# Kernel tuning notes

Measured on AMD Instinct MI355X. Metric: run time of the kernel, lower is better.

Reference implementation:

```python
import jax, jax.numpy as jnp
import numpy as np

DIM = 384; H = 56; W = 56; WS = 7; SHIFT = 3; NH = 12; B = 32
N = WS * WS                 # 49 tokens per window
NW = (H // WS) * (W // WS)  # 64 windows per image
HD = DIM // NH
EPS = 1e-5


def _rel_coords_table():
    c = np.arange(-(WS - 1), WS, dtype=np.float32)
    hh, ww = np.meshgrid(c, c, indexing='ij')
    t = np.stack([hh, ww], -1)[None]          # (1, 2*WS-1, 2*WS-1, 2)
    t = t / (WS - 1) * 8.0
    t = np.sign(t) * np.log2(np.abs(t) + 1.0) / 3.0
    return t.astype(np.float32)


def _rel_pos_index():
    coords = np.stack(np.meshgrid(np.arange(WS), np.arange(WS), indexing='ij'))  # (2,WS,WS)
    cf = coords.reshape(2, -1)
    rc = (cf[:, :, None] - cf[:, None, :]).transpose(1, 2, 0)  # (N,N,2)
    rc[..., 0] += WS - 1
    rc[..., 1] += WS - 1
    rc[..., 0] *= 2 * WS - 1
    return rc.sum(-1)  # (N,N) int


def _attn_mask():
    img = np.zeros((H, W))
    sl = [slice(0, -WS), slice(-WS, -SHIFT), slice(-SHIFT, None)]
    cnt = 0
    for hs in sl:
        for ws in sl:
            img[hs, ws] = cnt
            cnt += 1
    mw = img.reshape(H // WS, WS, W // WS, WS).transpose(0, 2, 1, 3).reshape(-1, N)
    diff = mw[:, None, :] - mw[:, :, None]  # (NW, N, N)
    return np.where(diff != 0, -100.0, 0.0).astype(np.float32)


_RCT = jnp.asarray(_rel_coords_table())
_RPI = jnp.asarray(_rel_pos_index().reshape(-1))
_MASK = jnp.asarray(_attn_mask())


def _layernorm(x, g, b):
    mu = jnp.mean(x, -1, keepdims=True)
    var = jnp.mean(jnp.square(x - mu), -1, keepdims=True)
    return (x - mu) * jax.lax.rsqrt(var + EPS) * g + b


def _forward(x, qkv_w, q_bias, v_bias, logit_scale, cpb_w1, cpb_b1, cpb_w2,
             proj_w, proj_b, norm1_g, norm1_b, norm2_g, norm2_b,
             mlp_w1, mlp_b1, mlp_w2, mlp_b2):
    shortcut = x
    xg = x.reshape(B, H, W, DIM)
    xg = jnp.roll(xg, shift=(-SHIFT, -SHIFT), axis=(1, 2))
    # window partition -> (B*NW, N, C)
    xw = xg.reshape(B, H // WS, WS, W // WS, WS, DIM).transpose(0, 1, 3, 2, 4, 5)
    xw = xw.reshape(B * NW, N, DIM)

    qkv_bias = jnp.concatenate([q_bias, jnp.zeros_like(v_bias), v_bias])
    qkv = xw @ qkv_w.T + qkv_bias                       # (Bw, N, 3C)
    qkv = qkv.reshape(B * NW, N, 3, NH, HD).transpose(2, 0, 3, 1, 4)
    q, k, v = qkv[0], qkv[1], qkv[2]                    # (Bw, NH, N, HD)

    qn = q / jnp.maximum(jnp.linalg.norm(q, axis=-1, keepdims=True), 1e-12)
    kn = k / jnp.maximum(jnp.linalg.norm(k, axis=-1, keepdims=True), 1e-12)
    attn = jnp.einsum('whnd,whmd->whnm', qn, kn)        # cosine attention
    scale = jnp.exp(jnp.minimum(logit_scale, jnp.log(100.0)))  # (NH,1,1)
    attn = attn * scale

    # CPB-MLP relative position bias
    bt = jnp.maximum(_RCT @ cpb_w1.T + cpb_b1, 0.0) @ cpb_w2.T  # (1,13,13,NH)
    bt = bt.reshape(-1, NH)
    rel_bias = bt[_RPI].reshape(N, N, NH).transpose(2, 0, 1)    # (NH,N,N)
    rel_bias = 16.0 * jax.nn.sigmoid(rel_bias)
    attn = attn + rel_bias[None]

    attn = attn.reshape(B, NW, NH, N, N) + _MASK[None, :, None]
    attn = jax.nn.softmax(attn, axis=-1).reshape(B * NW, NH, N, N)

    out = jnp.einsum('whnm,whmd->whnd', attn, v)        # (Bw, NH, N, HD)
    out = out.transpose(0, 2, 1, 3).reshape(B * NW, N, DIM)
    out = out @ proj_w.T + proj_b

    # window reverse + un-shift
    xg = out.reshape(B, H // WS, W // WS, WS, WS, DIM).transpose(0, 1, 3, 2, 4, 5)
    xg = xg.reshape(B, H, W, DIM)
    xg = jnp.roll(xg, shift=(SHIFT, SHIFT), axis=(1, 2))
    attn_out = xg.reshape(B, H * W, DIM)

    # SwinV2 post-norm residuals
    x1 = shortcut + _layernorm(attn_out, norm1_g, norm1_b)
    h = jax.nn.gelu(x1 @ mlp_w1.T + mlp_b1, approximate=False) @ mlp_w2.T + mlp_b2
    return x1 + _layernorm(h, norm2_g, norm2_b)


def setup_inputs() -> dict:
    key = jax.random.key(0)
    ks = jax.random.split(key, 8)
    s = 0.02
    return {
        'x': jax.random.normal(ks[0], (B, H * W, DIM), jnp.float32),
        'qkv_w': jax.random.normal(ks[1], (3 * DIM, DIM), jnp.float32) * s,
        'q_bias': jnp.zeros((DIM,), jnp.float32),
        'v_bias': jnp.zeros((DIM,), jnp.float32),
        'logit_scale': jnp.log(10.0 * jnp.ones((NH, 1, 1), jnp.float32)),
        'cpb_w1': jax.random.normal(ks[2], (512, 2), jnp.float32) * s,
        'cpb_b1': jnp.zeros((512,), jnp.float32),
        'cpb_w2': jax.random.normal(ks[3], (NH, 512), jnp.float32) * s,
        'proj_w': jax.random.normal(ks[4], (DIM, DIM), jnp.float32) * s,
        'proj_b': jnp.zeros((DIM,), jnp.float32),
        'norm1_g': jnp.ones((DIM,), jnp.float32),
        'norm1_b': jnp.zeros((DIM,), jnp.float32),
        'norm2_g': jnp.ones((DIM,), jnp.float32),
        'norm2_b': jnp.zeros((DIM,), jnp.float32),
        'mlp_w1': jax.random.normal(ks[5], (4 * DIM, DIM), jnp.float32) * s,
        'mlp_b1': jnp.zeros((4 * DIM,), jnp.float32),
        'mlp_w2': jax.random.normal(ks[6], (DIM, 4 * DIM), jnp.float32) * s,
        'mlp_b2': jnp.zeros((DIM,), jnp.float32),
    }


def reference(x, qkv_w, q_bias, v_bias, logit_scale, cpb_w1, cpb_b1, cpb_w2,
              proj_w, proj_b, norm1_g, norm1_b, norm2_g, norm2_b,
              mlp_w1, mlp_b1, mlp_w2, mlp_b2):
    return _forward(x, qkv_w, q_bias, v_bias, logit_scale, cpb_w1, cpb_b1, cpb_w2,
                    proj_w, proj_b, norm1_g, norm1_b, norm2_g, norm2_b,
                    mlp_w1, mlp_b1, mlp_w2, mlp_b2)
```

## Files before the change

kernel.cpp:

```cpp
#include <hip/hip_runtime.h>
#include <hip/hip_bf16.h>
#include <math.h>

#define DIM 384
#define NH 12
#define HD 32
#define NWIN 2048
#define TOKENS 100352
#define NSTG 6

typedef unsigned short u16;
typedef unsigned int u32;
typedef __attribute__((ext_vector_type(8))) short bf16x8;
typedef __attribute__((ext_vector_type(4))) float f32x4;

__device__ __forceinline__ float b2f(u16 u){ return __uint_as_float(((u32)u) << 16); }
__device__ __forceinline__ u16 f2b(float f){
  u32 x = __float_as_uint(f);
  return (u16)((x + 0x7FFFu + ((x >> 16) & 1u)) >> 16);
}

__device__ __forceinline__ void gld16(void* lds, const void* g){
  __builtin_amdgcn_global_load_lds((const __attribute__((address_space(1))) u32*)g,
                                   (__attribute__((address_space(3))) u32*)lds, 16, 0, 0);
}

__global__ void k_wconv(const float* __restrict__ w1, const float* __restrict__ w2,
                        const float* __restrict__ qw, const float* __restrict__ pw,
                        u16* __restrict__ w1s, u16* __restrict__ w2s,
                        u16* __restrict__ qwbf, u16* __restrict__ pws){
  const int n12 = 1536*384, n3 = 1152*384, n4 = 384*384;
  for (int d = blockIdx.x*blockDim.x + threadIdx.x; d < n12; d += gridDim.x*blockDim.x){
    int tile = d >> 12, w = d & 4095;
    int rowl = w >> 5, g = (w >> 3) & 3, e = w & 7;
    int hci = tile / 12, rem = tile - hci*12;
    int kk = ((g ^ (rowl & 3)) << 3) + e;
    w1s[d] = f2b(w1[(size_t)(hci*128 + rowl)*384 + rem*32 + kk]);
    int ks = rem / 3, t = rem - ks*3;
    w2s[d] = f2b(w2[(size_t)(t*128 + rowl)*1536 + hci*128 + ks*32 + kk]);
    if (d < n3) qwbf[d] = f2b(qw[d]);
    if (d < n4){
      int pt = d >> 12, pwd = d & 4095;
      int prl = pwd >> 5, pg = (pwd >> 3) & 3, pe = pwd & 7;
      int pks = pt / 3, ptt = pt - pks*3;
      int pkk = ((pg ^ (prl & 3)) << 3) + pe;
      pws[d] = f2b(pw[(size_t)(ptt*128 + prl)*384 + pks*32 + pkk]);
    }
  }
}

__global__ void k_bias(const float* __restrict__ w1, const float* __restrict__ b1,
                       const float* __restrict__ w2, float* __restrict__ tab){
  __shared__ float hid[512];
  int e = blockIdx.x;
  int i = e / 13, j = e % 13;
  float t0 = (float)(i - 6) * (8.0f / 6.0f);
  float t1 = (float)(j - 6) * (8.0f / 6.0f);
  t0 = copysignf(log2f(fabsf(t0) + 1.f) * (1.f / 3.f), t0);
  t1 = copysignf(log2f(fabsf(t1) + 1.f) * (1.f / 3.f), t1);
  for (int jj = threadIdx.x; jj < 512; jj += blockDim.x)
    hid[jj] = fmaxf(w1[jj*2]*t0 + w1[jj*2+1]*t1 + b1[jj], 0.f);
  __syncthreads();
  if (threadIdx.x < 12){
    float s = 0.f;
    for (int jj = 0; jj < 512; ++jj) s += hid[jj] * w2[threadIdx.x*512 + jj];
    tab[e*12 + threadIdx.x] = s;
  }
}

__global__ void k_bias2(const float* __restrict__ tab, float* __restrict__ biasfull){
  int h = blockIdx.x;
  for (int e = threadIdx.x; e < 49*49; e += blockDim.x){
    int i = e / 49, j = e - (e/49)*49;
    int ih = i/7, iw = i - ih*7, jh = j/7, jw = j - jh*7;
    float bv = tab[((ih-jh+6)*13 + (iw-jw+6))*12 + h];
    biasfull[h*2401 + e] = 16.f / (1.f + expf(-bv));
  }
}

__device__ __forceinline__ void qkv_stage(
    int kc, char* Ad, char* Bd, const float* __restrict__ x, size_t asrc,
    bool arok, int ar, int aq, const u16* __restrict__ bbase, int tid){
  if (arok){
    float4 v4 = *(const float4*)(x + asrc + kc + aq*4);
    u16 p0=f2b(v4.x), p1=f2b(v4.y), p2=f2b(v4.z), p3=f2b(v4.w);
    *(uint2*)(Ad + ar*80 + aq*8) = (uint2){(u32)p0|((u32)p1<<16), (u32)p2|((u32)p3<<16)};
  } else {
    *(uint2*)(Ad + ar*80 + aq*8) = (uint2){0u, 0u};
  }
  #pragma unroll
  for (int i = 0; i < 3; ++i){
    int s = tid + i*512, n = s >> 2, g = s & 3;
    bf16x8 v = *(const bf16x8*)(bbase + (size_t)n*DIM + kc + (g ^ (n&3))*8);
    *(bf16x8*)(Bd + n*64 + g*16) = v;
  }
}

__global__ __launch_bounds__(512, 4) void k_qkv(
    const float* __restrict__ x, const u16* __restrict__ qkvbf,
    const float* __restrict__ q_bias, const float* __restrict__ v_bias,
    const float* __restrict__ logit_scale,
    u16* __restrict__ Qg, u16* __restrict__ Kg, u16* __restrict__ Vg){
  __shared__ __align__(16) char Ab[2][5120];
  __shared__ __align__(16) char Bb[2][24576];

  int tid = threadIdx.x;
  int lane = tid & 63, wid = tid >> 6;
  int l15 = lane & 15, lg = lane >> 4;
  int wm = wid >> 2, wn = wid & 3;
  int win = blockIdx.x, NT = blockIdx.y;
  int b = win >> 6, wi = win & 63, wh = wi >> 3, ww = wi & 7;

  int ar = tid >> 3, aq = tid & 7;
  bool arok = ar < 49;
  size_t asrc = 0;
  if (arok){
    int th = ar / 7, tw = ar - (ar/7)*7;
    int gh = wh*7 + th + 3; if (gh >= 56) gh -= 56;
    int gw = ww*7 + tw + 3; if (gw >= 56) gw -= 56;
    asrc = ((size_t)(b*3136 + gh*56 + gw))*DIM;
  }
  const u16* bbase = qkvbf + (size_t)NT*384*DIM;

  f32x4 acc[2][6];
  #pragma unroll
  for (int mf = 0; mf < 2; ++mf)
    #pragma unroll
    for (int nf = 0; nf < 6; ++nf) acc[mf][nf] = (f32x4){0.f,0.f,0.f,0.f};

  qkv_stage(0, Ab[0], Bb[0], x, asrc, arok, ar, aq, bbase, tid);
  __syncthreads();

  for (int t = 0; t < 12; ++t){
    int cur = t & 1;
    if (t < 11)
      qkv_stage((t+1)*32, Ab[cur^1], Bb[cur^1], x, asrc, arok, ar, aq, bbase, tid);
    bf16x8 af[2];
    #pragma unroll
    for (int mf = 0; mf < 2; ++mf){
      int row = wm*32 + mf*16 + l15;
      af[mf] = *(const bf16x8*)(Ab[cur] + row*80 + lg*16);
    }
    #pragma unroll
    for (int nf = 0; nf < 6; ++nf){
      int n = wn*96 + nf*16 + l15;
      bf16x8 bfv = *(const bf16x8*)(Bb[cur] + n*64 + ((lg ^ (n&3))*16));
      #pragma unroll
      for (int mf = 0; mf < 2; ++mf)
        acc[mf][nf] = __builtin_amdgcn_mfma_f32_16x16x32_bf16(af[mf], bfv, acc[mf][nf], 0, 0, 0);
    }
    __syncthreads();
  }

  if (NT == 0){
    #pragma unroll
    for (int p = 0; p < 3; ++p){
      int h = wn*3 + p;
      float qb0 = q_bias[h*32 + l15], qb1 = q_bias[h*32 + 16 + l15];
      float sc = __expf(fminf(logit_scale[h], 4.6051702f));
      #pragma unroll
      for (int mf = 0; mf < 2; ++mf)
        #pragma unroll
        for (int r = 0; r < 4; ++r){
          float a0 = acc[mf][2*p][r] + qb0;
          float a1 = acc[mf][2*p+1][r] + qb1;
          float sq = a0*a0 + a1*a1;
          #pragma unroll
          for (int off = 1; off < 16; off <<= 1) sq += __shfl_xor(sq, off, 64);
          float rq = sc / fmaxf(sqrtf(sq), 1e-12f);
          int grow = wm*32 + mf*16 + lg*4 + r;
          if (grow < 49){
            u16* dst = Qg + (size_t)win*18816 + h*1568 + grow*32;
            dst[l15]      = f2b(a0*rq);
            dst[16 + l15] = f2b(a1*rq);
          }
        }
    }
  } else if (NT == 1){
    #pragma unroll
    for (int p = 0; p < 3; ++p){
      int h = wn*3 + p;
      #pragma unroll
      for (int mf = 0; mf < 2; ++mf)
        #pragma unroll
        for (int r = 0; r < 4; ++r){
          float a0 = acc[mf][2*p][r], a1 = acc[mf][2*p+1][r];
          float sk = a0*a0 + a1*a1;
          #pragma unroll
          for (int off = 1; off < 16; off <<= 1) sk += __shfl_xor(sk, off, 64);
          float rk = 1.f / fmaxf(sqrtf(sk), 1e-12f);
          int grow = wm*32 + mf*16 + lg*4 + r;
          if (grow < 49){
            u16* dst = Kg + (size_t)win*18816 + h*1568 + grow*32;
            dst[l15]      = f2b(a0*rk);
            dst[16 + l15] = f2b(a1*rk);
          }
        }
    }
  } else {
    #pragma unroll
    for (int nf = 0; nf < 6; ++nf){
      int col = wn*96 + nf*16 + l15;
      int h = col >> 5, c = col & 31;
      float vb = v_bias[col];
      #pragma unroll
      for (int mf = 0; mf < 2; ++mf){
        int gbase = wm*32 + mf*16 + lg*4;
        u16* dst = Vg + (size_t)win*18816 + h*1568 + c;
        #pragma unroll
        for (int r = 0; r < 4; ++r){
          int grow = gbase + r;
          if (grow < 49) dst[grow*32] = f2b(acc[mf][nf][r] + vb);
        }
      }
    }
  }
}

__global__ __launch_bounds__(256, 3) void k_attn2(
    const u16* __restrict__ Qg, const u16* __restrict__ Kg, const u16* __restrict__ Vg,
    const float* __restrict__ biasfull, u16* __restrict__ outwin){
  __shared__ __align__(16) char pb[4][2304];

  int tid = threadIdx.x, lane = tid & 63, wid = tid >> 6;
  int l15 = lane & 15, lg = lane >> 4;
  int win = blockIdx.x;
  int wi = win & 63, wh = wi >> 3, ww = wi & 7;

  float mask16[4][4];
  int   bidx[4][4];
  #pragma unroll
  for (int nf = 0; nf < 4; ++nf){
    int j = nf*16 + l15;
    int j2 = j < 49 ? j : 48;
    int jh = j2/7, jw = j2 - jh*7;
    int ghj = wh*7+jh, gwj = ww*7+jw;
    int zj = (ghj<49?0:(ghj<53?1:2))*3 + (gwj<49?0:(gwj<53?1:2));
    #pragma unroll
    for (int r = 0; r < 4; ++r){
      int i = wid*16 + lg*4 + r;
      int i2 = i < 49 ? i : 48;
      int ih = i2/7, iw = i2 - ih*7;
      int ghi = wh*7+ih, gwi = ww*7+iw;
      int zi = (ghi<49?0:(ghi<53?1:2))*3 + (gwi<49?0:(gwi<53?1:2));
      mask16[nf][r] = (j < 49) ? (zi != zj ? -100.f : 0.f) : -1e30f;
      bidx[nf][r]   = i2*49 + j2;
    }
  }

  const u16* qwin = Qg + (size_t)win*18816;
  const u16* kwin = Kg + (size_t)win*18816;
  const u16* vwin = Vg + (size_t)win*18816;
  char* pbw = pb[wid];

  int arow = wid*16 + l15;
  int arc  = arow < 49 ? arow : 48;

  bf16x8 qa[12];
  #pragma unroll
  for (int h = 0; h < 12; ++h)
    qa[h] = *(const bf16x8*)(qwin + h*1568 + arc*32 + lg*8);
  __syncthreads();

  #pragma unroll
  for (int h = 0; h < 12; ++h){
    bf16x8 kb[4];
    #pragma unroll
    for (int nf = 0; nf < 4; ++nf){
      int j = nf*16 + l15; int j2 = j < 49 ? j : 48;
      kb[nf] = *(const bf16x8*)(kwin + h*1568 + j2*32 + lg*8);
    }
    bf16x8 vb0[2], vb1[2];
    #pragma unroll
    for (int ksp = 0; ksp < 2; ++ksp){
      #pragma unroll
      for (int tt = 0; tt < 8; ++tt){
        int j = ksp*32 + lg*8 + tt; int j2 = j < 49 ? j : 48;
        vb0[ksp][tt] = (short)vwin[h*1568 + j2*32 + l15];
        vb1[ksp][tt] = (short)vwin[h*1568 + j2*32 + 16 + l15];
      }
    }
    float bias16[4][4];
    #pragma unroll
    for (int nf = 0; nf < 4; ++nf)
      #pragma unroll
      for (int r = 0; r < 4; ++r)
        bias16[nf][r] = biasfull[h*2401 + bidx[nf][r]];
    f32x4 s[4];
    #pragma unroll
    for (int nf = 0; nf < 4; ++nf)
      s[nf] = __builtin_amdgcn_mfma_f32_16x16x32_bf16(qa[h], kb[nf],
                (f32x4){0.f,0.f,0.f,0.f}, 0, 0, 0);
    #pragma unroll
    for (int nf = 0; nf < 4; ++nf)
      #pragma unroll
      for (int r = 0; r < 4; ++r)
        s[nf][r] += bias16[nf][r] + mask16[nf][r];
    #pragma unroll
    for (int r = 0; r < 4; ++r){
      float m = fmaxf(fmaxf(s[0][r], s[1][r]), fmaxf(s[2][r], s[3][r]));
      #pragma unroll
      for (int off = 1; off < 16; off <<= 1) m = fmaxf(m, __shfl_xor(m, off, 64));
      float e0 = __expf(s[0][r]-m), e1 = __expf(s[1][r]-m);
      float e2 = __expf(s[2][r]-m), e3 = __expf(s[3][r]-m);
      float sum = e0+e1+e2+e3;
      #pragma unroll
      for (int off = 1; off < 16; off <<= 1) sum += __shfl_xor(sum, off, 64);
      float rs = 1.f/sum;
      s[0][r] = e0*rs; s[1][r] = e1*rs; s[2][r] = e2*rs; s[3][r] = e3*rs;
    }
    #pragma unroll
    for (int nf = 0; nf < 4; ++nf){
      int j = nf*16 + l15;
      #pragma unroll
      for (int r = 0; r < 4; ++r)
        *(u16*)(pbw + (lg*4+r)*144 + j*2) = f2b(s[nf][r]);
    }
    f32x4 o0 = (f32x4){0.f,0.f,0.f,0.f}, o1 = o0;
    #pragma unroll
    for (int ksp = 0; ksp < 2; ++ksp){
      bf16x8 pa = *(const bf16x8*)(pbw + l15*144 + ksp*64 + lg*16);
      o0 = __builtin_amdgcn_mfma_f32_16x16x32_bf16(pa, vb0[ksp], o0, 0, 0, 0);
      o1 = __builtin_amdgcn_mfma_f32_16x16x32_bf16(pa, vb1[ksp], o1, 0, 0, 0);
    }
    #pragma unroll
    for (int r = 0; r < 4; ++r){
      int row = wid*16 + lg*4 + r;
      if (row < 49){
        u16* dst = outwin + ((size_t)win*49 + row)*DIM + h*HD;
        dst[l15]      = f2b(o0[r]);
        dst[16 + l15] = f2b(o1[r]);
      }
    }
  }
}

__global__ __launch_bounds__(512, 2) void k_proj(
    const u16* __restrict__ outwin, const u16* __restrict__ pws,
    const float* __restrict__ proj_b, const float* __restrict__ x,
    const float* __restrict__ n1g, const float* __restrict__ n1b,
    float* __restrict__ x1){
  extern __shared__ char smem[];
  char* sb = smem;
  char* Wb = smem + 49152;

  int tid  = threadIdx.x;
  int lane = tid & 63, wid = tid >> 6;
  int l15  = lane & 15, lg = lane >> 4;
  int gt0 = blockIdx.x * 64;

  for (int e = tid; e < 64*48; e += 512){
    int r = e / 48, q8 = e - (e/48)*48;
    int gtok = gt0 + r;
    int b = gtok / 3136, r2 = gtok - b*3136;
    int oh = r2 / 56, ow = r2 - oh*56;
    int hs = oh + 53; if (hs >= 56) hs -= 56;
    int ws2 = ow + 53; if (ws2 >= 56) ws2 -= 56;
    int win = b*64 + (hs/7)*8 + (ws2/7);
    int row = (hs%7)*7 + (ws2%7);
    bf16x8 v = *(const bf16x8*)(outwin + ((size_t)win*49 + row)*DIM + q8*8);
    *(bf16x8*)(sb + r*768 + ((q8*16) ^ ((r&15)<<4))) = v;
  }

  f32x4 acc[4][3];
  #pragma unroll
  for (int mf = 0; mf < 4; ++mf)
    #pragma unroll
    for (int t = 0; t < 3; ++t){
      float pbv = proj_b[(wid + 8*t)*16 + l15];
      acc[mf][t] = (f32x4){pbv, pbv, pbv, pbv};
    }

  int goff = tid*16;
  int rowl = wid*16 + l15;
  int wswz = (lg ^ (rowl&3)) << 4;
  #pragma unroll
  for (int sp = 0; sp < NSTG-1; ++sp)
    gld16(Wb + sp*8192 + wid*1024, (const char*)pws + (size_t)sp*8192 + goff);
  __syncthreads();

  #pragma unroll
  for (int ks = 0; ks < 12; ++ks){
    int k0 = ks*32 + lg*8;
    bf16x8 pa[4];
    #pragma unroll
    for (int mf = 0; mf < 4; ++mf){
      int row = mf*16 + l15;
      pa[mf] = *(const bf16x8*)(sb + row*768 + ((k0*2) ^ ((row&15)<<4)));
    }
    #pragma unroll
    for (int t = 0; t < 3; ++t){
      int st = ks*3 + t;
      asm volatile("s_waitcnt vmcnt(4)" ::: "memory");
      __builtin_amdgcn_sched_barrier(0);
      {
        int rp = st + 5;
        char* dst = Wb + ((st+5)%6)*8192 + wid*1024;
        if (rp < 36) gld16(dst, (const char*)pws + (size_t)rp*8192 + goff);
        else         gld16(dst, (const char*)pws + goff);
      }
      char* Wcur = Wb + (st%6)*8192;
      bf16x8 wv = *(const bf16x8*)(Wcur + rowl*64 + wswz);
      #pragma unroll
      for (int mf = 0; mf < 4; ++mf)
        acc[mf][t] = __builtin_amdgcn_mfma_f32_16x16x32_bf16(pa[mf], wv, acc[mf][t], 0, 0, 0);
    }
  }
  __syncthreads();

  float* part = (float*)Wb;
  float* lnf  = (float*)(Wb + 4096);
  float s1a[4][4], s2a[4][4];
  #pragma unroll
  for (int mf = 0; mf < 4; ++mf)
    #pragma unroll
    for (int r = 0; r < 4; ++r){
      float p1 = acc[mf][0][r] + acc[mf][1][r] + acc[mf][2][r];
      float p2 = acc[mf][0][r]*acc[mf][0][r] + acc[mf][1][r]*acc[mf][1][r]
               + acc[mf][2][r]*acc[mf][2][r];
      #pragma unroll
      for (int off = 1; off < 16; off <<= 1){
        p1 += __shfl_xor(p1, off, 64);
        p2 += __shfl_xor(p2, off, 64);
      }
      s1a[mf][r] = p1; s2a[mf][r] = p2;
    }
  if (l15 == 0){
    #pragma unroll
    for (int mf = 0; mf < 4; ++mf)
      #pragma unroll
      for (int r = 0; r < 4; ++r){
        int row = mf*16 + lg*4 + r;
        part[(row*8 + wid)*2]     = s1a[mf][r];
        part[(row*8 + wid)*2 + 1] = s2a[mf][r];
      }
  }
  __syncthreads();
  if (tid < 64){
    float t1 = 0.f, t2 = 0.f;
    #pragma unroll
    for (int w = 0; w < 8; ++w){
      t1 += part[(tid*8 + w)*2];
      t2 += part[(tid*8 + w)*2 + 1];
    }
    float mu = t1*(1.f/384.f);
    lnf[tid*2]     = mu;
    lnf[tid*2 + 1] = rsqrtf(t2*(1.f/384.f) - mu*mu + 1e-5f);
  }
  __syncthreads();
  #pragma unroll
  for (int mf = 0; mf < 4; ++mf)
    #pragma unroll
    for (int r = 0; r < 4; ++r){
      int row = mf*16 + lg*4 + r;
      float mu = lnf[row*2], rstd = lnf[row*2 + 1];
      #pragma unroll
      for (int t = 0; t < 3; ++t){
        int col = (wid + 8*t)*16 + l15;
        x1[(size_t)(gt0 + row)*DIM + col] =
            (acc[mf][t][r]-mu)*rstd*n1g[col] + n1b[col] + x[(size_t)(gt0 + row)*DIM + col];
      }
    }
}

__global__ __launch_bounds__(512, 4) void k_mlp(
    const float* __restrict__ x1, const u16* __restrict__ w1s, const float* __restrict__ b1,
    const u16* __restrict__ w2s, const float* __restrict__ b2,
    const float* __restrict__ n2g, const float* __restrict__ n2b,
    float* __restrict__ out){
  extern __shared__ char smem[];
  char* xb = smem;
  char* Wb = smem + 24576;
  char* hb = smem + 24576 + 49152;

  int tid  = threadIdx.x;
  int lane = tid & 63, wid = tid >> 6;
  int l15  = lane & 15, lg = lane >> 4;
  int gt0 = blockIdx.x * 32;

  for (int e = tid; e < 32*48; e += 512){
    int r = e / 48, q8 = e - (e/48)*48;
    const float4* src = (const float4*)(x1 + (size_t)(gt0+r)*DIM + q8*8);
    float4 a = src[0], c = src[1];
    bf16x8 v;
    v[0]=(short)f2b(a.x); v[1]=(short)f2b(a.y); v[2]=(short)f2b(a.z); v[3]=(short)f2b(a.w);
    v[4]=(short)f2b(c.x); v[5]=(short)f2b(c.y); v[6]=(short)f2b(c.z); v[7]=(short)f2b(c.w);
    *(bf16x8*)(xb + r*768 + ((q8*16) ^ ((r&15)<<4))) = v;
  }
  int b1c = wid*16 + l15;
  float b1r0 = b1[b1c],          b1r1 = b1[128 + b1c],  b1r2 = b1[256 + b1c];
  float b1r3 = b1[384 + b1c],    b1r4 = b1[512 + b1c],  b1r5 = b1[640 + b1c];
  float b1r6 = b1[768 + b1c],    b1r7 = b1[896 + b1c],  b1r8 = b1[1024 + b1c];
  float b1r9 = b1[1152 + b1c],   b1r10 = b1[1280 + b1c], b1r11 = b1[1408 + b1c];

  f32x4 acc2[2][3];
  #pragma unroll
  for (int mf = 0; mf < 2; ++mf)
    #pragma unroll
    for (int t = 0; t < 3; ++t){
      float bb = b2[(wid + 8*t)*16 + l15];
      acc2[mf][t] = (f32x4){bb, bb, bb, bb};
    }

  int goff = tid*16;
  int rowl = wid*16 + l15;
  int wswz = (lg ^ (rowl&3)) << 4;
  #pragma unroll
  for (int sp = 0; sp < NSTG-1; ++sp)
    gld16(Wb + sp*8192 + wid*1024, (const char*)w1s + (size_t)sp*8192 + goff);
  __syncthreads();

  for (int hci = 0; hci < 12; ++hci){
    const char* w1c = (const char*)w1s + (size_t)hci*98304;
    const char* w2c = (const char*)w2s + (size_t)hci*98304;
    const char* w1n = (const char*)w1s + (size_t)(hci+1)*98304;

    float bb = hci==0?b1r0 : hci==1?b1r1 : hci==2?b1r2 : hci==3?b1r3 :
               hci==4?b1r4 : hci==5?b1r5 : hci==6?b1r6 : hci==7?b1r7 :
               hci==8?b1r8 : hci==9?b1r9 : hci==10?b1r10 : b1r11;
    f32x4 accH[2];
    #pragma unroll
    for (int mf = 0; mf < 2; ++mf) accH[mf] = (f32x4){bb, bb, bb, bb};

    #pragma unroll
    for (int ksp = 0; ksp < 12; ++ksp){
      asm volatile("s_waitcnt vmcnt(4)" ::: "memory");
      __builtin_amdgcn_sched_barrier(0);
      {
        int rp = ksp + 5;
        char* dst = Wb + ((ksp+5)%6)*8192 + wid*1024;
        const char* src = (rp < 12) ? (w1c + (size_t)rp*8192)
                                    : (w2c + (size_t)(rp-12)*8192);
        gld16(dst, src + goff);
      }
      char* Wcur = Wb + (ksp%6)*8192;
      int k0 = ksp*32 + lg*8;
      bf16x8 wfr = *(const bf16x8*)(Wcur + rowl*64 + wswz);
      bf16x8 afr[2];
      #pragma unroll
      for (int mf = 0; mf < 2; ++mf){
        int row = mf*16 + l15;
        afr[mf] = *(const bf16x8*)(xb + row*768 + ((k0*2) ^ ((row&15)<<4)));
      }
      #pragma unroll
      for (int mf = 0; mf < 2; ++mf)
        accH[mf] = __builtin_amdgcn_mfma_f32_16x16x32_bf16(afr[mf], wfr, accH[mf], 0, 0, 0);
    }

    #pragma unroll
    for (int mf = 0; mf < 2; ++mf)
      #pragma unroll
      for (int r = 0; r < 4; ++r){
        float v = accH[mf][r];
        v = 0.5f*v*(1.f + erff(v*0.70710678f));
        int row = mf*16 + lg*4 + r;
        int col = wid*16 + l15;
        *(u16*)(hb + row*256 + ((col*2) ^ ((row&15)<<4))) = f2b(v);
      }
    asm volatile("s_waitcnt lgkmcnt(0)" ::: "memory");
    __builtin_amdgcn_s_barrier();
    __builtin_amdgcn_sched_barrier(0);

    #pragma unroll
    for (int ks = 0; ks < 4; ++ks){
      int k0 = ks*32 + lg*8;
      bf16x8 pa[2];
      #pragma unroll
      for (int mf = 0; mf < 2; ++mf){
        int row = mf*16 + l15;
        pa[mf] = *(const bf16x8*)(hb + row*256 + ((k0*2) ^ ((row&15)<<4)));
      }
      #pragma unroll
      for (int t = 0; t < 3; ++t){
        int st = ks*3 + t;
        asm volatile("s_waitcnt vmcnt(4)" ::: "memory");
        __builtin_amdgcn_sched_barrier(0);
        {
          int rp = st + 17;
          char* dst = Wb + ((st+5)%6)*8192 + wid*1024;
          if (rp < 24)       gld16(dst, w2c + (size_t)(rp-12)*8192 + goff);
          else if (hci < 11) gld16(dst, w1n + (size_t)(rp-24)*8192 + goff);
          else               gld16(dst, (const char*)w1s + goff);
        }
        char* Wcur = Wb + (st%6)*8192;
        bf16x8 wv = *(const bf16x8*)(Wcur + rowl*64 + wswz);
        #pragma unroll
        for (int mf = 0; mf < 2; ++mf)
          acc2[mf][t] = __builtin_amdgcn_mfma_f32_16x16x32_bf16(pa[mf], wv, acc2[mf][t], 0, 0, 0);
      }
    }
    asm volatile("s_waitcnt lgkmcnt(0)" ::: "memory");
    __builtin_amdgcn_s_barrier();
    __builtin_amdgcn_sched_barrier(0);
  }
  __syncthreads();

  float* part = (float*)hb;
  float* lnf  = (float*)(hb + 2048);
  float s1a[2][4], s2a[2][4];
  #pragma unroll
  for (int mf = 0; mf < 2; ++mf)
    #pragma unroll
    for (int r = 0; r < 4; ++r){
      float p1 = acc2[mf][0][r] + acc2[mf][1][r] + acc2[mf][2][r];
      float p2 = acc2[mf][0][r]*acc2[mf][0][r] + acc2[mf][1][r]*acc2[mf][1][r]
               + acc2[mf][2][r]*acc2[mf][2][r];
      #pragma unroll
      for (int off = 1; off < 16; off <<= 1){
        p1 += __shfl_xor(p1, off, 64);
        p2 += __shfl_xor(p2, off, 64);
      }
      s1a[mf][r] = p1; s2a[mf][r] = p2;
    }
  if (l15 == 0){
    #pragma unroll
    for (int mf = 0; mf < 2; ++mf)
      #pragma unroll
      for (int r = 0; r < 4; ++r){
        int row = mf*16 + lg*4 + r;
        part[(row*8 + wid)*2]     = s1a[mf][r];
        part[(row*8 + wid)*2 + 1] = s2a[mf][r];
      }
  }
  __syncthreads();
  if (tid < 32){
    float t1 = 0.f, t2 = 0.f;
    #pragma unroll
    for (int w = 0; w < 8; ++w){
      t1 += part[(tid*8 + w)*2];
      t2 += part[(tid*8 + w)*2 + 1];
    }
    float mu = t1*(1.f/384.f);
    lnf[tid*2]     = mu;
    lnf[tid*2 + 1] = rsqrtf(t2*(1.f/384.f) - mu*mu + 1e-5f);
  }
  __syncthreads();
  #pragma unroll
  for (int mf = 0; mf < 2; ++mf)
    #pragma unroll
    for (int r = 0; r < 4; ++r){
      int row = mf*16 + lg*4 + r;
      float mu = lnf[row*2], rstd = lnf[row*2 + 1];
      #pragma unroll
      for (int t = 0; t < 3; ++t){
        int col = (wid + 8*t)*16 + l15;
        float resid = x1[(size_t)(gt0 + row)*DIM + col];
        out[(size_t)(gt0 + row)*DIM + col] =
            resid + (acc2[mf][t][r]-mu)*rstd*n2g[col] + n2b[col];
      }
    }
}

extern "C" void kernel_launch(void* const* d_in, const int* in_sizes, int n_in,
                              void* d_out, int out_size, void* d_ws, size_t ws_size,
                              hipStream_t stream){
  const float* x           = (const float*)d_in[0];
  const float* qkv_w       = (const float*)d_in[1];
  const float* q_bias      = (const float*)d_in[2];
  const float* v_bias      = (const float*)d_in[3];
  const float* logit_scale = (const float*)d_in[4];
  const float* cpb_w1      = (const float*)d_in[5];
  const float* cpb_b1      = (const float*)d_in[6];
  const float* cpb_w2      = (const float*)d_in[7];
  const float* proj_w      = (const float*)d_in[8];
  const float* proj_b      = (const float*)d_in[9];
  const float* n1g         = (const float*)d_in[10];
  const float* n1b         = (const float*)d_in[11];
  const float* n2g         = (const float*)d_in[12];
  const float* n2b         = (const float*)d_in[13];
  const float* mlp_w1      = (const float*)d_in[14];
  const float* mlp_b1      = (const float*)d_in[15];
  const float* mlp_w2      = (const float*)d_in[16];
  const float* mlp_b2      = (const float*)d_in[17];

  char* ws = (char*)d_ws;
  float* tab      = (float*)ws;
  float* biasfull = (float*)(ws + 8192);
  u16*  Qg     = (u16*)(ws + 126976);
  u16*  qkvbf  = (u16*)(ws + 126976 + 77070336ull);
  u16*  pws    = (u16*)(ws + 126976 + 77070336ull + 884736ull);
  u16*  w1s    = (u16*)(ws + 126976 + 77070336ull + 884736ull + 294912ull);
  u16*  w2s    = (u16*)(ws + 126976 + 77070336ull + 884736ull + 294912ull + 1179648ull);
  u16*  Kg     = (u16*)d_out;
  u16*  Vg     = Kg + (size_t)NWIN*18816;
  u16*  outwin = Qg;
  float* x1  = (float*)d_out;
  float* out = (float*)d_out;

  hipLaunchKernelGGL(k_bias, dim3(169), dim3(256), 0, stream, cpb_w1, cpb_b1, cpb_w2, tab);
  hipLaunchKernelGGL(k_bias2, dim3(12), dim3(256), 0, stream, tab, biasfull);
  hipLaunchKernelGGL(k_wconv, dim3(1024), dim3(256), 0, stream,
                     mlp_w1, mlp_w2, qkv_w, proj_w, w1s, w2s, qkvbf, pws);
  hipLaunchKernelGGL(k_qkv, dim3(NWIN, 3), dim3(512), 0, stream,
                     x, qkvbf, q_bias, v_bias, logit_scale, Qg, Kg, Vg);
  hipLaunchKernelGGL(k_attn2, dim3(NWIN), dim3(256), 0, stream,
                     Qg, Kg, Vg, biasfull, outwin);
  hipLaunchKernelGGL(k_proj, dim3(TOKENS/64), dim3(512), 98304, stream,
                     outwin, pws, proj_b, x, n1g, n1b, x1);
  hipLaunchKernelGGL(k_mlp, dim3(TOKENS/32), dim3(512), 81920, stream,
                     x1, w1s, mlp_b1, w2s, mlp_b2, n2g, n2b, out);
}
```

Measured before the change: 1.020 ms.

## Restructure QKV GEMM with resident x tile and async weight pipeline; tanh GELU

The QKV kernel now loads the whole 49x384 window input into swizzled LDS once and streams pre-tiled bf16 weights through a 6-stage global_load_lds ring buffer, processing output in three column groups of four heads each. The weight conversion kernel writes QKV weights in a tiled, swizzled layout to match. This aims to cut per-step synchronisation and the repeated fp32-to-bf16 conversion latency on the critical path, at the cost of 96KB dynamic LDS and lower occupancy (launch bounds 512,2). Separately, the MLP GELU swaps exact erf for a tanh approximation expressed via exp and a fast reciprocal, which changes numerics slightly.

Measured after the change: 1.092 ms. 1.07x slower.

```diff
diff --git a/kernel.cpp b/kernel.cpp
--- a/kernel.cpp
+++ b/kernel.cpp
@@ -28,7 +28,7 @@
 __global__ void k_wconv(const float* __restrict__ w1, const float* __restrict__ w2,
                         const float* __restrict__ qw, const float* __restrict__ pw,
                         u16* __restrict__ w1s, u16* __restrict__ w2s,
-                        u16* __restrict__ qwbf, u16* __restrict__ pws){
+                        u16* __restrict__ qkvs, u16* __restrict__ pws){
   const int n12 = 1536*384, n3 = 1152*384, n4 = 384*384;
   for (int d = blockIdx.x*blockDim.x + threadIdx.x; d < n12; d += gridDim.x*blockDim.x){
     int tile = d >> 12, w = d & 4095;
@@ -38,7 +38,8 @@
     w1s[d] = f2b(w1[(size_t)(hci*128 + rowl)*384 + rem*32 + kk]);
     int ks = rem / 3, t = rem - ks*3;
     w2s[d] = f2b(w2[(size_t)(t*128 + rowl)*1536 + hci*128 + ks*32 + kk]);
-    if (d < n3) qwbf[d] = f2b(qw[d]);
+    if (d < n3)
+      qkvs[d] = f2b(qw[(size_t)((tile/12)*128 + rowl)*384 + (tile%12)*32 + kk]);
     if (d < n4){
       int pt = d >> 12, pwd = d & 4095;
       int prl = pwd >> 5, pg = (pwd >> 3) & 3, pe = pwd & 7;
@@ -78,31 +79,14 @@
   }
 }
 
-__device__ __forceinline__ void qkv_stage(
-    int kc, char* Ad, char* Bd, const float* __restrict__ x, size_t asrc,
-    bool arok, int ar, int aq, const u16* __restrict__ bbase, int tid){
-  if (arok){
-    float4 v4 = *(const float4*)(x + asrc + kc + aq*4);
-    u16 p0=f2b(v4.x), p1=f2b(v4.y), p2=f2b(v4.z), p3=f2b(v4.w);
-    *(uint2*)(Ad + ar*80 + aq*8) = (uint2){(u32)p0|((u32)p1<<16), (u32)p2|((u32)p3<<16)};
-  } else {
-    *(uint2*)(Ad + ar*80 + aq*8) = (uint2){0u, 0u};
-  }
-  #pragma unroll
-  for (int i = 0; i < 3; ++i){
-    int s = tid + i*512, n = s >> 2, g = s & 3;
-    bf16x8 v = *(const bf16x8*)(bbase + (size_t)n*DIM + kc + (g ^ (n&3))*8);
-    *(bf16x8*)(Bd + n*64 + g*16) = v;
-  }
-}
-
-__global__ __launch_bounds__(512, 4) void k_qkv(
-    const float* __restrict__ x, const u16* __restrict__ qkvbf,
+__global__ __launch_bounds__(512, 2) void k_qkv(
+    const float* __restrict__ x, const u16* __restrict__ qkvs,
     const float* __restrict__ q_bias, const float* __restrict__ v_bias,
     const float* __restrict__ logit_scale,
     u16* __restrict__ Qg, u16* __restrict__ Kg, u16* __restrict__ Vg){
-  __shared__ __align__(16) char Ab[2][5120];
-  __shared__ __align__(16) char Bb[2][24576];
+  extern __shared__ char smem[];
+  char* xb = smem;
+  char* Wb = smem + 49152;
 
   int tid = threadIdx.x;
   int lane = tid & 63, wid = tid >> 6;
@@ -111,59 +95,78 @@
   int win = blockIdx.x, NT = blockIdx.y;
   int b = win >> 6, wi = win & 63, wh = wi >> 3, ww = wi & 7;
 
-  int ar = tid >> 3, aq = tid & 7;
-  bool arok = ar < 49;
-  size_t asrc = 0;
-  if (arok){
-    int th = ar / 7, tw = ar - (ar/7)*7;
-    int gh = wh*7 + th + 3; if (gh >= 56) gh -= 56;
-    int gw = ww*7 + tw + 3; if (gw >= 56) gw -= 56;
-    asrc = ((size_t)(b*3136 + gh*56 + gw))*DIM;
-  }
-  const u16* bbase = qkvbf + (size_t)NT*384*DIM;
-
-  f32x4 acc[2][6];
-  #pragma unroll
-  for (int mf = 0; mf < 2; ++mf)
-    #pragma unroll
-    for (int nf = 0; nf < 6; ++nf) acc[mf][nf] = (f32x4){0.f,0.f,0.f,0.f};
-
-  qkv_stage(0, Ab[0], Bb[0], x, asrc, arok, ar, aq, bbase, tid);
-  __syncthreads();
-
-  for (int t = 0; t < 12; ++t){
-    int cur = t & 1;
-    if (t < 11)
-      qkv_stage((t+1)*32, Ab[cur^1], Bb[cur^1], x, asrc, arok, ar, aq, bbase, tid);
-    bf16x8 af[2];
-    #pragma unroll
-    for (int mf = 0; mf < 2; ++mf){
-      int row = wm*32 + mf*16 + l15;
-      af[mf] = *(const bf16x8*)(Ab[cur] + row*80 + lg*16);
-    }
-    #pragma unroll
-    for (int nf = 0; nf < 6; ++nf){
-      int n = wn*96 + nf*16 + l15;
-      bf16x8 bfv = *(const bf16x8*)(Bb[cur] + n*64 + ((lg ^ (n&3))*16));
+  for (int e = tid; e < 64*48; e += 512){
+    int r = e / 48, q8 = e - (e/48)*48;
+    bf16x8 v = (bf16x8){0,0,0,0,0,0,0,0};
+    if (r < 49){
+      int th = r / 7, tw = r - (r/7)*7;
+      int gh = wh*7 + th + 3; if (gh >= 56) gh -= 56;
+      int gw = ww*7 + tw + 3; if (gw >= 56) gw -= 56;
+      const float4* src = (const float4*)(x + ((size_t)(b*3136 + gh*56 + gw))*DIM + q8*8);
+      float4 a = src[0], c = src[1];
+      v[0]=(short)f2b(a.x); v[1]=(short)f2b(a.y); v[2]=(short)f2b(a.z); v[3]=(short)f2b(a.w);
+      v[4]=(short)f2b(c.x); v[5]=(short)f2b(c.y); v[6]=(short)f2b(c.z); v[7]=(short)f2b(c.w);
+    }
+    *(bf16x8*)(xb + r*768 + ((q8*16) ^ ((r&15)<<4))) = v;
+  }
+
+  const char* tb = (const char*)qkvs + (size_t)NT*36*8192;
+  int goff = tid*16;
+  #pragma unroll
+  for (int sp = 0; sp < NSTG-1; ++sp)
+    gld16(Wb + sp*8192 + wid*1024, tb + (size_t)sp*8192 + goff);
+  __syncthreads();
+
+  for (int cg = 0; cg < 3; ++cg){
+    f32x4 acc[2][2];
+    #pragma unroll
+    for (int mf = 0; mf < 2; ++mf)
+      #pragma unroll
+      for (int nf = 0; nf < 2; ++nf) acc[mf][nf] = (f32x4){0.f,0.f,0.f,0.f};
+
+    #pragma unroll
+    for (int ksp = 0; ksp < 12; ++ksp){
+      int st = cg*12 + ksp;
+      asm volatile("s_waitcnt vmcnt(4)" ::: "memory");
+      __builtin_amdgcn_s_barrier();
+      __builtin_amdgcn_sched_barrier(0);
+      {
+        int rp = st + 5;
+        char* dst = Wb + ((st+5)%6)*8192 + wid*1024;
+        if (rp < 36) gld16(dst, tb + (size_t)rp*8192 + goff);
+        else         gld16(dst, tb + goff);
+      }
+      char* Wcur = Wb + (st%6)*8192;
+      int k0 = ksp*32 + lg*8;
+      bf16x8 bfv[2];
+      #pragma unroll
+      for (int nf = 0; nf < 2; ++nf){
+        int row = wn*32 + nf*16 + l15;
+        bfv[nf] = *(const bf16x8*)(Wcur + row*64 + ((lg ^ (row&3))<<4));
+      }
+      bf16x8 af[2];
+      #pragma unroll
+      for (int mf = 0; mf < 2; ++mf){
+        int row = wm*32 + mf*16 + l15;
+        af[mf] = *(const bf16x8*)(xb + row*768 + ((k0*2) ^ ((row&15)<<4)));
+      }
       #pragma unroll
       for (int mf = 0; mf < 2; ++mf)
-        acc[mf][nf] = __builtin_amdgcn_mfma_f32_16x16x32_bf16(af[mf], bfv, acc[mf][nf], 0, 0, 0);
-    }
-    __syncthreads();
-  }
-
-  if (NT == 0){
-    #pragma unroll
-    for (int p = 0; p < 3; ++p){
-      int h = wn*3 + p;
+        #pragma unroll
+        for (int nf = 0; nf < 2; ++nf)
+          acc[mf][nf] = __builtin_amdgcn_mfma_f32_16x16x32_bf16(af[mf], bfv[nf], acc[mf][nf], 0, 0, 0);
+    }
+
+    int h = cg*4 + wn;
+    if (NT == 0){
       float qb0 = q_bias[h*32 + l15], qb1 = q_bias[h*32 + 16 + l15];
       float sc = __expf(fminf(logit_scale[h], 4.6051702f));
       #pragma unroll
       for (int mf = 0; mf < 2; ++mf)
         #pragma unroll
         for (int r = 0; r < 4; ++r){
-          float a0 = acc[mf][2*p][r] + qb0;
-          float a1 = acc[mf][2*p+1][r] + qb1;
+          float a0 = acc[mf][0][r] + qb0;
+          float a1 = acc[mf][1][r] + qb1;
           float sq = a0*a0 + a1*a1;
           #pragma unroll
           for (int off = 1; off < 16; off <<= 1) sq += __shfl_xor(sq, off, 64);
@@ -175,16 +178,12 @@
             dst[16 + l15] = f2b(a1*rq);
           }
         }
-    }
-  } else if (NT == 1){
-    #pragma unroll
-    for (int p = 0; p < 3; ++p){
-      int h = wn*3 + p;
+    } else if (NT == 1){
       #pragma unroll
       for (int mf = 0; mf < 2; ++mf)
         #pragma unroll
         for (int r = 0; r < 4; ++r){
-          float a0 = acc[mf][2*p][r], a1 = acc[mf][2*p+1][r];
+          float a0 = acc[mf][0][r], a1 = acc[mf][1][r];
           float sk = a0*a0 + a1*a1;
           #pragma unroll
           for (int off = 1; off < 16; off <<= 1) sk += __shfl_xor(sk, off, 64);
@@ -196,24 +195,23 @@
             dst[16 + l15] = f2b(a1*rk);
           }
         }
-    }
-  } else {
-    #pragma unroll
-    for (int nf = 0; nf < 6; ++nf){
-      int col = wn*96 + nf*16 + l15;
-      int h = col >> 5, c = col & 31;
-      float vb = v_bias[col];
-      #pragma unroll
-      for (int mf = 0; mf < 2; ++mf){
-        int gbase = wm*32 + mf*16 + lg*4;
-        u16* dst = Vg + (size_t)win*18816 + h*1568 + c;
+    } else {
+      float vb0 = v_bias[h*32 + l15], vb1 = v_bias[h*32 + 16 + l15];
+      #pragma unroll
+      for (int mf = 0; mf < 2; ++mf)
         #pragma unroll
         for (int r = 0; r < 4; ++r){
-          int grow = gbase + r;
-          if (grow < 49) dst[grow*32] = f2b(acc[mf][nf][r] + vb);
+          int grow = wm*32 + mf*16 + lg*4 + r;
+          if (grow < 49){
+            u16* dst = Vg + (size_t)win*18816 + h*1568 + grow*32;
+            dst[l15]      = f2b(acc[mf][0][r] + vb0);
+            dst[16 + l15] = f2b(acc[mf][1][r] + vb1);
+          }
         }
-      }
-    }
+    }
+    asm volatile("s_waitcnt vmcnt(0)" ::: "memory");
+    __builtin_amdgcn_s_barrier();
+    __builtin_amdgcn_sched_barrier(0);
   }
 }
 
@@ -552,7 +550,8 @@
       #pragma unroll
       for (int r = 0; r < 4; ++r){
         float v = accH[mf][r];
-        v = 0.5f*v*(1.f + erff(v*0.70710678f));
+        float u = v*(1.f + 0.044715f*v*v);
+        v = v * __builtin_amdgcn_rcpf(1.f + __expf(-1.5957691f*u));
         int row = mf*16 + lg*4 + r;
         int col = wid*16 + l15;
         *(u16*)(hb + row*256 + ((col*2) ^ ((row&15)<<4))) = f2b(v);
@@ -677,7 +676,7 @@
   float* tab      = (float*)ws;
   float* biasfull = (float*)(ws + 8192);
   u16*  Qg     = (u16*)(ws + 126976);
-  u16*  qkvbf  = (u16*)(ws + 126976 + 77070336ull);
+  u16*  qkvs   = (u16*)(ws + 126976 + 77070336ull);
   u16*  pws    = (u16*)(ws + 126976 + 77070336ull + 884736ull);
   u16*  w1s    = (u16*)(ws + 126976 + 77070336ull + 884736ull + 294912ull);
   u16*  w2s    = (u16*)(ws + 126976 + 77070336ull + 884736ull + 294912ull + 1179648ull);
@@ -690,9 +689,9 @@
   hipLaunchKernelGGL(k_bias, dim3(169), dim3(256), 0, stream, cpb_w1, cpb_b1, cpb_w2, tab);
   hipLaunchKernelGGL(k_bias2, dim3(12), dim3(256), 0, stream, tab, biasfull);
   hipLaunchKernelGGL(k_wconv, dim3(1024), dim3(256), 0, stream,
-                     mlp_w1, mlp_w2, qkv_w, proj_w, w1s, w2s, qkvbf, pws);
-  hipLaunchKernelGGL(k_qkv, dim3(NWIN, 3), dim3(512), 0, stream,
-                     x, qkvbf, q_bias, v_bias, logit_scale, Qg, Kg, Vg);
+                     mlp_w1, mlp_w2, qkv_w, proj_w, w1s, w2s, qkvs, pws);
+  hipLaunchKernelGGL(k_qkv, dim3(NWIN, 3), dim3(512), 98304, stream,
+                     x, qkvs, q_bias, v_bias, logit_scale, Qg, Kg, Vg);
   hipLaunchKernelGGL(k_attn2, dim3(NWIN), dim3(256), 0, stream,
                      Qg, Kg, Vg, biasfull, outwin);
   hipLaunchKernelGGL(k_proj, dim3(TOKENS/64), dim3(512), 98304, stream,
```
